# Kernel tuning notes

Measured on AMD Instinct MI355X. Metric: run time of the kernel, lower is better.

## Reference

```python
import jax, jax.numpy as jnp
import numpy as np
import math

SIG = 0.3989422804014327  # 1/sqrt(2*pi): makes sqrt_pi == 1, matching init_kwargs
N = 4000002


def _toeplitz_like_t(c):
    # Faithful result of toeplitz_like(x,5).t() for x=[1,N]:
    # full Toeplitz T[i,j]=c[|i-j|], narrow(1,0,2).narrow(0,1,N-2).t()
    # => rows are shifted windows c[1:N-1] and c[0:N-2], shape [2, N-2].
    n = c.shape[0]
    return jnp.stack([c[1:n - 1], c[0:n - 2]], axis=0)


def _component(A, B, log_sqrt_pi):
    # A, B: [M, D].  sum_{i,j,k} exp(-0.5*(A[i,k]-B[j,k])^2/sig^2)/sqrt_pi / (M*M)
    M = A.shape[0]
    diff = A[:, None, :] - B[None, :, :]          # [M, M, D]
    g = jnp.exp(-0.5 * (diff * diff) / (SIG * SIG) - log_sqrt_pi)
    return jnp.sum(g) / (M * M)


def setup_inputs() -> dict:
    key = jax.random.key(0)
    k1, k2 = jax.random.split(key)
    d = jax.random.normal(k1, (N,), dtype=jnp.float32)
    y = jax.random.normal(k2, (N,), dtype=jnp.float32)
    return {"d": d, "y": y}


def reference(d, y):
    Dm = _toeplitz_like_t(d)                      # [2, N-2]
    Ym = _toeplitz_like_t(y)                      # [2, N-2]
    Ddim = Ym.shape[1]
    # sqrt_pi = sqrt((2*pi)^D * sig^(2D)); computed stably in log space
    log_sqrt_pi = 0.5 * Ddim * (math.log(2.0 * math.pi) + 2.0 * math.log(SIG))
    log_sqrt_pi = jnp.float32(log_sqrt_pi)
    same_y = _component(Ym, Ym, log_sqrt_pi)
    same_d = _component(Dm, Dm, log_sqrt_pi)
    combined = -2.0 * _component(Dm, Ym, log_sqrt_pi)
    return same_y + same_d + combined
```

## Files before the change

kernel.cpp:

```cpp
#include <hip/hip_runtime.h>


#define PI_F 3.14159265358979323846f
#define NBLOCKS 1024
#define FINAL_THREADS 1024

__device__ __forceinline__ float six_terms(float d0, float d1, float y0, float y1) {
    float dy = y1 - y0;
    float dd = d1 - d0;
    float c00 = d1 - y1;
    float c01 = d1 - y0;
    float c10 = d0 - y1;
    float c11 = d0 - y0;
    return __expf(-PI_F * dy * dy) + __expf(-PI_F * dd * dd)
         - __expf(-PI_F * c00 * c00) - __expf(-PI_F * c01 * c01)
         - __expf(-PI_F * c10 * c10) - __expf(-PI_F * c11 * c11);
}

__global__ __launch_bounds__(256) void casamento_partial(
    const float* __restrict__ d, const float* __restrict__ y,
    float* __restrict__ ws, int D)
{
    int tid = blockIdx.x * blockDim.x + threadIdx.x;
    int stride = gridDim.x * blockDim.x;
    int D4 = D >> 2;

    float acc = 0.0f;
    for (int u = tid; u < D4; u += stride) {
        int base = u << 2;
        float4 dv = *(const float4*)(d + base);
        float4 yv = *(const float4*)(y + base);
        float d4 = d[base + 4];
        float y4 = y[base + 4];

        acc += six_terms(dv.x, dv.y, yv.x, yv.y);
        acc += six_terms(dv.y, dv.z, yv.y, yv.z);
        acc += six_terms(dv.z, dv.w, yv.z, yv.w);
        acc += six_terms(dv.w, d4,   yv.w, y4);
    }

    if (tid == 0) {
        for (int k = (D4 << 2); k < D; ++k)
            acc += six_terms(d[k], d[k + 1], y[k], y[k + 1]);
    }

    acc *= 0.5f;

    for (int off = 32; off > 0; off >>= 1)
        acc += __shfl_down(acc, off, 64);

    __shared__ float warp_sums[4];
    int lane = threadIdx.x & 63;
    int wid  = threadIdx.x >> 6;
    if (lane == 0) warp_sums[wid] = acc;
    __syncthreads();

    if (threadIdx.x == 0)
        ws[blockIdx.x] = warp_sums[0] + warp_sums[1] + warp_sums[2] + warp_sums[3];
}

__global__ __launch_bounds__(FINAL_THREADS) void casamento_final(
    const float* __restrict__ ws, float* __restrict__ out, int D)
{
    float acc = (threadIdx.x < NBLOCKS) ? ws[threadIdx.x] : 0.0f;

    for (int off = 32; off > 0; off >>= 1)
        acc += __shfl_down(acc, off, 64);

    __shared__ float warp_sums[FINAL_THREADS / 64];
    int lane = threadIdx.x & 63;
    int wid  = threadIdx.x >> 6;
    if (lane == 0) warp_sums[wid] = acc;
    __syncthreads();

    if (threadIdx.x == 0) {
        float s = 0.0f;
        #pragma unroll
        for (int i = 0; i < FINAL_THREADS / 64; ++i) s += warp_sums[i];
        out[0] = s + (float)D;
    }
}

extern "C" void kernel_launch(void* const* d_in, const int* in_sizes, int n_in,
                              void* d_out, int out_size, void* d_ws, size_t ws_size,
                              hipStream_t stream) {
    const float* d = (const float*)d_in[0];
    const float* y = (const float*)d_in[1];
    float* out = (float*)d_out;
    float* ws  = (float*)d_ws;

    int N = in_sizes[0];
    int D = N - 2;

    casamento_partial<<<NBLOCKS, 256, 0, stream>>>(d, y, ws, D);
    casamento_final<<<1, FINAL_THREADS, 0, stream>>>(ws, out, D);
}
```

Measured before the change: 75.58 us.

## Launch one thread per 8-element chunk instead of a grid-stride loop

Replaces the fixed 1024-block grid-stride loop with a grid sized to the data, where each thread handles exactly 8 consecutive positions using two float4 loads per input. The final reduction kernel now loops over a variable number of block partials (about 1954). The intent is more blocks in flight to hide memory latency and more independent exp work per thread. The cost is a larger partial array for the final pass to reduce.

```diff
diff --git a/kernel.cpp b/kernel.cpp
--- a/kernel.cpp
+++ b/kernel.cpp
@@ -2,7 +2,8 @@
 
 
 #define PI_F 3.14159265358979323846f
-#define NBLOCKS 1024
+#define NTHREADS 256
+#define ELEMS_PER_THREAD 8
 #define FINAL_THREADS 1024
 
 __device__ __forceinline__ float six_terms(float d0, float d1, float y0, float y1) {
@@ -17,30 +18,32 @@
          - __expf(-PI_F * c10 * c10) - __expf(-PI_F * c11 * c11);
 }
 
-__global__ __launch_bounds__(256) void casamento_partial(
+__global__ __launch_bounds__(NTHREADS) void casamento_partial(
     const float* __restrict__ d, const float* __restrict__ y,
     float* __restrict__ ws, int D)
 {
-    int tid = blockIdx.x * blockDim.x + threadIdx.x;
-    int stride = gridDim.x * blockDim.x;
-    int D4 = D >> 2;
+    int gtid = blockIdx.x * NTHREADS + threadIdx.x;
+    int base = gtid * ELEMS_PER_THREAD;
 
     float acc = 0.0f;
-    for (int u = tid; u < D4; u += stride) {
-        int base = u << 2;
-        float4 dv = *(const float4*)(d + base);
-        float4 yv = *(const float4*)(y + base);
-        float d4 = d[base + 4];
-        float y4 = y[base + 4];
+    if (base + ELEMS_PER_THREAD <= D) {
+        float4 a = *(const float4*)(d + base);
+        float4 b = *(const float4*)(d + base + 4);
+        float4 p = *(const float4*)(y + base);
+        float4 q = *(const float4*)(y + base + 4);
+        float d8 = d[base + 8];
+        float y8 = y[base + 8];
 
-        acc += six_terms(dv.x, dv.y, yv.x, yv.y);
-        acc += six_terms(dv.y, dv.z, yv.y, yv.z);
-        acc += six_terms(dv.z, dv.w, yv.z, yv.w);
-        acc += six_terms(dv.w, d4,   yv.w, y4);
-    }
-
-    if (tid == 0) {
-        for (int k = (D4 << 2); k < D; ++k)
+        acc += six_terms(a.x, a.y, p.x, p.y);
+        acc += six_terms(a.y, a.z, p.y, p.z);
+        acc += six_terms(a.z, a.w, p.z, p.w);
+        acc += six_terms(a.w, b.x, p.w, q.x);
+        acc += six_terms(b.x, b.y, q.x, q.y);
+        acc += six_terms(b.y, b.z, q.y, q.z);
+        acc += six_terms(b.z, b.w, q.z, q.w);
+        acc += six_terms(b.w, d8,  q.w, y8);
+    } else if (base < D) {
+        for (int k = base; k < D; ++k)
             acc += six_terms(d[k], d[k + 1], y[k], y[k + 1]);
     }
 
@@ -49,7 +52,7 @@
     for (int off = 32; off > 0; off >>= 1)
         acc += __shfl_down(acc, off, 64);
 
-    __shared__ float warp_sums[4];
+    __shared__ float warp_sums[NTHREADS / 64];
     int lane = threadIdx.x & 63;
     int wid  = threadIdx.x >> 6;
     if (lane == 0) warp_sums[wid] = acc;
@@ -60,9 +63,11 @@
 }
 
 __global__ __launch_bounds__(FINAL_THREADS) void casamento_final(
-    const float* __restrict__ ws, float* __restrict__ out, int D)
+    const float* __restrict__ ws, float* __restrict__ out, int D, int NB)
 {
-    float acc = (threadIdx.x < NBLOCKS) ? ws[threadIdx.x] : 0.0f;
+    float acc = 0.0f;
+    for (int i = threadIdx.x; i < NB; i += FINAL_THREADS)
+        acc += ws[i];
 
     for (int off = 32; off > 0; off >>= 1)
         acc += __shfl_down(acc, off, 64);
@@ -92,6 +97,9 @@
     int N = in_sizes[0];
     int D = N - 2;
 
-    casamento_partial<<<NBLOCKS, 256, 0, stream>>>(d, y, ws, D);
-    casamento_final<<<1, FINAL_THREADS, 0, stream>>>(ws, out, D);
+    int units = (D + ELEMS_PER_THREAD - 1) / ELEMS_PER_THREAD;
+    int NB = (units + NTHREADS - 1) / NTHREADS;
+
+    casamento_partial<<<NB, NTHREADS, 0, stream>>>(d, y, ws, D);
+    casamento_final<<<1, FINAL_THREADS, 0, stream>>>(ws, out, D, NB);
 }
```

New measurement: 75.87 us. No clear change (+0.4%).
